# Kernel optimization log

Hardware: AMD Instinct MI355X
Metric: run time of the kernel (lower is better)

The kernel has to match this reference:

```python
import jax, jax.numpy as jnp
import numpy as np

DT = 0.2
LEN_HIST = 16
BATCH = 100000
LEN_PRED = 25


def _consts():
    H = jnp.zeros((2, 4), jnp.float32).at[0, 0].set(1.0).at[1, 2].set(1.0)
    Ht = H.T
    F = jnp.eye(4, dtype=jnp.float32).at[0, 1].set(DT).at[2, 3].set(DT)
    G = jnp.array([DT * DT / 2, DT, DT * DT / 2, DT], dtype=jnp.float32)
    Id = jnp.eye(4, dtype=jnp.float32)
    return H, Ht, F, G, Id


def setup_inputs():
    key = jax.random.key(0)
    hist = jax.random.normal(key, (LEN_HIST, BATCH, 2), dtype=jnp.float32)
    return {
        "hist": hist,
        "velocity_std_x": jnp.ones((1,), jnp.float32) * 0.1355,
        "velocity_std_y": jnp.ones((1,), jnp.float32) * 20.007,
        "acceleration_std_x": jnp.ones((1,), jnp.float32) * 2.771,
        "acceleration_std_y": jnp.ones((1,), jnp.float32) * 6.2014,
        "GR": jnp.array([1e-5, -1e-5], jnp.float32),
        "coef_G": jnp.array([-2.5296, 0.0723, -0.1533, -0.4032], jnp.float32),
        "len_pred": LEN_PRED,
    }


def _forward(hist, vsx, vsy, asx, asy, GR, coef_G, len_pred):
    H, Ht, F, G, Id = _consts()
    # Process noise Q: outer(G*tanh(coef_G)) with x/y diagonal blocks scaled
    ax2 = (asx * asx)[0]
    ay2 = (asy * asy)[0]
    mx = jnp.array([1.0, 1.0, 0.0, 0.0], jnp.float32)
    my = 1.0 - mx
    scale = ax2 * jnp.outer(mx, mx) + ay2 * jnp.outer(my, my) + jnp.outer(mx, my) + jnp.outer(my, mx)
    g = G * jnp.tanh(coef_G)
    Q = jnp.outer(g, g) * scale  # (4,4)
    R = jnp.outer(GR, GR)        # (2,2) measurement noise

    Z = hist[..., None]          # (T, B, 2, 1)
    B = hist.shape[1]

    # --- init ---
    V0 = (Z[1] - Z[0]) / DT                      # (B,2,1)
    X = Ht @ Z[0]                                # (B,4,1)
    X = X.at[:, 1, 0].set(V0[:, 0, 0]).at[:, 3, 0].set(V0[:, 1, 0])
    diag0 = jnp.stack([R[0, 0], (vsx * vsx)[0], R[1, 1], (vsy * vsy)[0]])
    P = jnp.broadcast_to(jnp.diag(diag0), (B, 4, 4))

    def pred(X, P):
        return F @ X, F @ P @ F.T + Q

    def filt_step(carry, z):
        X, P = carry
        X, P = pred(X, P)
        y = z - H @ X                            # (B,2,1)
        S = H @ P @ Ht + R                       # (B,2,2)
        # K = P H^T S^{-1}, computed as in torch.solve(H P^T, S^T)^T
        Kt = jnp.linalg.solve(jnp.swapaxes(S, -1, -2), H @ jnp.swapaxes(P, -1, -2))
        K = jnp.swapaxes(Kt, -1, -2)             # (B,4,2)
        X = X + K @ y
        ImKH = Id - K @ H
        P = ImKH @ P @ jnp.swapaxes(ImKH, -1, -2) + K @ R @ jnp.swapaxes(K, -1, -2)
        return (X, P), None

    (X, P), _ = jax.lax.scan(filt_step, (X, P), Z[1:])

    def pred_step(carry, _):
        X, P = pred(*carry)
        mu = (H @ X)[..., 0]                     # (B,2)
        Pout = H @ P @ Ht                        # (B,2,2)
        return (X, P), (mu, Pout)

    _, (mu, Pout) = jax.lax.scan(pred_step, (X, P), None, length=len_pred)
    sx = jnp.sqrt(Pout[..., 0, 0])[..., None]    # (L,B,1)
    sy = jnp.sqrt(Pout[..., 1, 1])[..., None]
    rho = (Pout[..., 0, 1] + Pout[..., 1, 0])[..., None] / (2.0 * sx * sy)
    return jnp.concatenate([mu, sx, sy, rho], axis=2)  # (L,B,5)


def reference(hist, velocity_std_x, velocity_std_y, acceleration_std_x, acceleration_std_y, GR, coef_G, len_pred):
    return _forward(hist, velocity_std_x, velocity_std_y, acceleration_std_x,
                    acceleration_std_y, GR, coef_G, len_pred)
```

## Files before the change

### kernel.cpp

```cpp
#include <hip/hip_runtime.h>
#include <math.h>

#define DT 0.2f
#define LEN_HIST 16

__global__ __launch_bounds__(256) void kalman_cv_kernel(
    const float* __restrict__ hist,
    const float* __restrict__ vsx_p, const float* __restrict__ vsy_p,
    const float* __restrict__ asx_p, const float* __restrict__ asy_p,
    const float* __restrict__ GR_p,  const float* __restrict__ coefG_p,
    float* __restrict__ out, int B, int len_pred)
{
    int b = blockIdx.x * blockDim.x + threadIdx.x;
    if (b >= B) return;

    const float Gv0 = DT * DT * 0.5f, Gv1 = DT, Gv2 = DT * DT * 0.5f, Gv3 = DT;
    float ax2 = asx_p[0] * asx_p[0];
    float ay2 = asy_p[0] * asy_p[0];
    float g[4];
    g[0] = Gv0 * tanhf(coefG_p[0]);
    g[1] = Gv1 * tanhf(coefG_p[1]);
    g[2] = Gv2 * tanhf(coefG_p[2]);
    g[3] = Gv3 * tanhf(coefG_p[3]);
    float Q[4][4];
    #pragma unroll
    for (int i = 0; i < 4; ++i) {
        #pragma unroll
        for (int j = 0; j < 4; ++j) {
            float s = (i < 2) ? ((j < 2) ? ax2 : 1.0f)
                              : ((j < 2) ? 1.0f : ay2);
            Q[i][j] = g[i] * g[j] * s;
        }
    }
    float GR0 = GR_p[0], GR1 = GR_p[1];
    float R00 = GR0 * GR0, R01 = GR0 * GR1, R10 = GR1 * GR0, R11 = GR1 * GR1;
    float vsx2 = vsx_p[0] * vsx_p[0];
    float vsy2 = vsy_p[0] * vsy_p[0];

    float2 z[LEN_HIST];
    #pragma unroll
    for (int t = 0; t < LEN_HIST; ++t)
        z[t] = *reinterpret_cast<const float2*>(hist + ((size_t)t * B + b) * 2);

    float X0 = z[0].x;
    float X1 = (z[1].x - z[0].x) / DT;
    float X2 = z[0].y;
    float X3 = (z[1].y - z[0].y) / DT;

    float P[4][4] = {};
    P[0][0] = R00; P[1][1] = vsx2; P[2][2] = R11; P[3][3] = vsy2;

    #pragma unroll
    for (int t = 1; t < LEN_HIST; ++t) {
        X0 += DT * X1;
        X2 += DT * X3;
        float T[4][4];
        #pragma unroll
        for (int j = 0; j < 4; ++j) {
            T[0][j] = P[0][j] + DT * P[1][j];
            T[1][j] = P[1][j];
            T[2][j] = P[2][j] + DT * P[3][j];
            T[3][j] = P[3][j];
        }
        #pragma unroll
        for (int i = 0; i < 4; ++i) {
            P[i][0] = T[i][0] + DT * T[i][1] + Q[i][0];
            P[i][1] = T[i][1]               + Q[i][1];
            P[i][2] = T[i][2] + DT * T[i][3] + Q[i][2];
            P[i][3] = T[i][3]               + Q[i][3];
        }

        float y0 = z[t].x - X0;
        float y1 = z[t].y - X2;
        float S00 = P[0][0] + R00, S01 = P[0][2] + R01;
        float S10 = P[2][0] + R10, S11 = P[2][2] + R11;
        float inv = 1.0f / (S00 * S11 - S01 * S10);
        float Si00 =  S11 * inv, Si01 = -S01 * inv;
        float Si10 = -S10 * inv, Si11 =  S00 * inv;

        float K[4][2];
        #pragma unroll
        for (int i = 0; i < 4; ++i) {
            K[i][0] = P[i][0] * Si00 + P[i][2] * Si10;
            K[i][1] = P[i][0] * Si01 + P[i][2] * Si11;
        }

        X0 += K[0][0] * y0 + K[0][1] * y1;
        X1 += K[1][0] * y0 + K[1][1] * y1;
        X2 += K[2][0] * y0 + K[2][1] * y1;
        X3 += K[3][0] * y0 + K[3][1] * y1;

        float U[4][4];
        #pragma unroll
        for (int i = 0; i < 4; ++i) {
            #pragma unroll
            for (int j = 0; j < 4; ++j)
                U[i][j] = P[i][j] - K[i][0] * P[0][j] - K[i][1] * P[2][j];
        }
        float w[4];
        #pragma unroll
        for (int i = 0; i < 4; ++i)
            w[i] = K[i][0] * GR0 + K[i][1] * GR1;
        #pragma unroll
        for (int i = 0; i < 4; ++i) {
            #pragma unroll
            for (int j = 0; j < 4; ++j)
                P[i][j] = U[i][j] - U[i][0] * K[j][0] - U[i][2] * K[j][1] + w[i] * w[j];
        }
    }

    size_t ob = (size_t)b * 5;
    for (int l = 0; l < len_pred; ++l) {
        X0 += DT * X1;
        X2 += DT * X3;
        float T[4][4];
        #pragma unroll
        for (int j = 0; j < 4; ++j) {
            T[0][j] = P[0][j] + DT * P[1][j];
            T[1][j] = P[1][j];
            T[2][j] = P[2][j] + DT * P[3][j];
            T[3][j] = P[3][j];
        }
        #pragma unroll
        for (int i = 0; i < 4; ++i) {
            P[i][0] = T[i][0] + DT * T[i][1] + Q[i][0];
            P[i][1] = T[i][1]               + Q[i][1];
            P[i][2] = T[i][2] + DT * T[i][3] + Q[i][2];
            P[i][3] = T[i][3]               + Q[i][3];
        }
        float sx = sqrtf(P[0][0]);
        float sy = sqrtf(P[2][2]);
        float rho = (P[0][2] + P[2][0]) / (2.0f * sx * sy);
        float* o = out + (size_t)l * B * 5 + ob;
        o[0] = X0;
        o[1] = X2;
        o[2] = sx;
        o[3] = sy;
        o[4] = rho;
    }
}

extern "C" void kernel_launch(void* const* d_in, const int* in_sizes, int n_in,
                              void* d_out, int out_size, void* d_ws, size_t ws_size,
                              hipStream_t stream) {
    const float* hist  = (const float*)d_in[0];
    const float* vsx   = (const float*)d_in[1];
    const float* vsy   = (const float*)d_in[2];
    const float* asx   = (const float*)d_in[3];
    const float* asy   = (const float*)d_in[4];
    const float* GR    = (const float*)d_in[5];
    const float* coefG = (const float*)d_in[6];
    float* out = (float*)d_out;

    int B = in_sizes[0] / (LEN_HIST * 2);
    int len_pred = out_size / (B * 5);

    int block = 256;
    int grid = (B + block - 1) / block;
    kalman_cv_kernel<<<grid, block, 0, stream>>>(hist, vsx, vsy, asx, asy, GR, coefG,
                                                 out, B, len_pred);
}
```

Measured before the change: 26.72 us.

## Exploit covariance symmetry and simplify Joseph update to reduce per-step ALU work

Stores the 4x4 covariance as its 10 unique upper-triangular entries and expands the F P F^T + Q product symbolically. The Joseph-form covariance update is replaced by the simple (I-KH)P form. Together these cut the FLOPs and register pressure of each filter and prediction step. The (I-KH)P form is mathematically equal only for the optimal gain and is less numerically robust, so results may drift slightly from the reference.

Measured after the change: 23.66 us. 1.13x faster.

```diff
diff --git a/kernel.cpp b/kernel.cpp
--- a/kernel.cpp
+++ b/kernel.cpp
@@ -3,140 +3,113 @@
 
 #define DT 0.2f
 #define LEN_HIST 16
+#define TPB 256
 
-__global__ __launch_bounds__(256) void kalman_cv_kernel(
+__global__ __launch_bounds__(TPB) void kalman_v4(
     const float* __restrict__ hist,
     const float* __restrict__ vsx_p, const float* __restrict__ vsy_p,
     const float* __restrict__ asx_p, const float* __restrict__ asy_p,
     const float* __restrict__ GR_p,  const float* __restrict__ coefG_p,
     float* __restrict__ out, int B, int len_pred)
 {
-    int b = blockIdx.x * blockDim.x + threadIdx.x;
+    const int b = blockIdx.x * TPB + threadIdx.x;
     if (b >= B) return;
-
-    const float Gv0 = DT * DT * 0.5f, Gv1 = DT, Gv2 = DT * DT * 0.5f, Gv3 = DT;
-    float ax2 = asx_p[0] * asx_p[0];
-    float ay2 = asy_p[0] * asy_p[0];
-    float g[4];
-    g[0] = Gv0 * tanhf(coefG_p[0]);
-    g[1] = Gv1 * tanhf(coefG_p[1]);
-    g[2] = Gv2 * tanhf(coefG_p[2]);
-    g[3] = Gv3 * tanhf(coefG_p[3]);
-    float Q[4][4];
-    #pragma unroll
-    for (int i = 0; i < 4; ++i) {
-        #pragma unroll
-        for (int j = 0; j < 4; ++j) {
-            float s = (i < 2) ? ((j < 2) ? ax2 : 1.0f)
-                              : ((j < 2) ? 1.0f : ay2);
-            Q[i][j] = g[i] * g[j] * s;
-        }
-    }
-    float GR0 = GR_p[0], GR1 = GR_p[1];
-    float R00 = GR0 * GR0, R01 = GR0 * GR1, R10 = GR1 * GR0, R11 = GR1 * GR1;
-    float vsx2 = vsx_p[0] * vsx_p[0];
-    float vsy2 = vsy_p[0] * vsy_p[0];
 
     float2 z[LEN_HIST];
     #pragma unroll
     for (int t = 0; t < LEN_HIST; ++t)
         z[t] = *reinterpret_cast<const float2*>(hist + ((size_t)t * B + b) * 2);
 
-    float X0 = z[0].x;
-    float X1 = (z[1].x - z[0].x) / DT;
-    float X2 = z[0].y;
-    float X3 = (z[1].y - z[0].y) / DT;
+    const float d = DT;
+    const float Gv0 = DT * DT * 0.5f, Gv1 = DT, Gv2 = DT * DT * 0.5f, Gv3 = DT;
+    const float ax2 = asx_p[0] * asx_p[0];
+    const float ay2 = asy_p[0] * asy_p[0];
+    const float g0 = Gv0 * tanhf(coefG_p[0]);
+    const float g1 = Gv1 * tanhf(coefG_p[1]);
+    const float g2 = Gv2 * tanhf(coefG_p[2]);
+    const float g3 = Gv3 * tanhf(coefG_p[3]);
+    const float Q00 = g0 * g0 * ax2, Q01 = g0 * g1 * ax2;
+    const float Q02 = g0 * g2,       Q03 = g0 * g3;
+    const float Q11 = g1 * g1 * ax2, Q12 = g1 * g2, Q13 = g1 * g3;
+    const float Q22 = g2 * g2 * ay2, Q23 = g2 * g3 * ay2, Q33 = g3 * g3 * ay2;
+    const float GR0 = GR_p[0], GR1 = GR_p[1];
+    const float R00 = GR0 * GR0, R01 = GR0 * GR1, R11 = GR1 * GR1;
 
-    float P[4][4] = {};
-    P[0][0] = R00; P[1][1] = vsx2; P[2][2] = R11; P[3][3] = vsy2;
+    float X0 = z[0].x, X1 = (z[1].x - z[0].x) / DT;
+    float X2 = z[0].y, X3 = (z[1].y - z[0].y) / DT;
+    float P00 = R00,                P01 = 0.f, P02 = 0.f, P03 = 0.f;
+    float P11 = vsx_p[0] * vsx_p[0], P12 = 0.f, P13 = 0.f;
+    float P22 = R11,                P23 = 0.f;
+    float P33 = vsy_p[0] * vsy_p[0];
 
     #pragma unroll
     for (int t = 1; t < LEN_HIST; ++t) {
-        X0 += DT * X1;
-        X2 += DT * X3;
-        float T[4][4];
-        #pragma unroll
-        for (int j = 0; j < 4; ++j) {
-            T[0][j] = P[0][j] + DT * P[1][j];
-            T[1][j] = P[1][j];
-            T[2][j] = P[2][j] + DT * P[3][j];
-            T[3][j] = P[3][j];
-        }
-        #pragma unroll
-        for (int i = 0; i < 4; ++i) {
-            P[i][0] = T[i][0] + DT * T[i][1] + Q[i][0];
-            P[i][1] = T[i][1]               + Q[i][1];
-            P[i][2] = T[i][2] + DT * T[i][3] + Q[i][2];
-            P[i][3] = T[i][3]               + Q[i][3];
-        }
+        const float n00 = P00 + d * (P01 + P01 + d * P11) + Q00;
+        const float n01 = P01 + d * P11 + Q01;
+        const float n02 = P02 + d * (P03 + P12 + d * P13) + Q02;
+        const float n03 = P03 + d * P13 + Q03;
+        const float n11 = P11 + Q11;
+        const float n12 = P12 + d * P13 + Q12;
+        const float n13 = P13 + Q13;
+        const float n22 = P22 + d * (P23 + P23 + d * P33) + Q22;
+        const float n23 = P23 + d * P33 + Q23;
+        const float n33 = P33 + Q33;
 
-        float y0 = z[t].x - X0;
-        float y1 = z[t].y - X2;
-        float S00 = P[0][0] + R00, S01 = P[0][2] + R01;
-        float S10 = P[2][0] + R10, S11 = P[2][2] + R11;
-        float inv = 1.0f / (S00 * S11 - S01 * S10);
-        float Si00 =  S11 * inv, Si01 = -S01 * inv;
-        float Si10 = -S10 * inv, Si11 =  S00 * inv;
+        X0 += d * X1; X2 += d * X3;
+        const float y0 = z[t].x - X0;
+        const float y1 = z[t].y - X2;
 
-        float K[4][2];
-        #pragma unroll
-        for (int i = 0; i < 4; ++i) {
-            K[i][0] = P[i][0] * Si00 + P[i][2] * Si10;
-            K[i][1] = P[i][0] * Si01 + P[i][2] * Si11;
-        }
+        const float S00 = n00 + R00, S01 = n02 + R01, S11 = n22 + R11;
+        const float inv = 1.0f / (S00 * S11 - S01 * S01);
+        const float Si00 = S11 * inv, Si01 = -S01 * inv, Si11 = S00 * inv;
 
-        X0 += K[0][0] * y0 + K[0][1] * y1;
-        X1 += K[1][0] * y0 + K[1][1] * y1;
-        X2 += K[2][0] * y0 + K[2][1] * y1;
-        X3 += K[3][0] * y0 + K[3][1] * y1;
+        const float K00 = n00 * Si00 + n02 * Si01, K01 = n00 * Si01 + n02 * Si11;
+        const float K10 = n01 * Si00 + n12 * Si01, K11 = n01 * Si01 + n12 * Si11;
+        const float K20 = n02 * Si00 + n22 * Si01, K21 = n02 * Si01 + n22 * Si11;
+        const float K30 = n03 * Si00 + n23 * Si01, K31 = n03 * Si01 + n23 * Si11;
 
-        float U[4][4];
-        #pragma unroll
-        for (int i = 0; i < 4; ++i) {
-            #pragma unroll
-            for (int j = 0; j < 4; ++j)
-                U[i][j] = P[i][j] - K[i][0] * P[0][j] - K[i][1] * P[2][j];
-        }
-        float w[4];
-        #pragma unroll
-        for (int i = 0; i < 4; ++i)
-            w[i] = K[i][0] * GR0 + K[i][1] * GR1;
-        #pragma unroll
-        for (int i = 0; i < 4; ++i) {
-            #pragma unroll
-            for (int j = 0; j < 4; ++j)
-                P[i][j] = U[i][j] - U[i][0] * K[j][0] - U[i][2] * K[j][1] + w[i] * w[j];
-        }
+        X0 += K00 * y0 + K01 * y1;
+        X1 += K10 * y0 + K11 * y1;
+        X2 += K20 * y0 + K21 * y1;
+        X3 += K30 * y0 + K31 * y1;
+
+        P00 = n00 - K00 * n00 - K01 * n02;
+        P01 = n01 - K00 * n01 - K01 * n12;
+        P02 = n02 - K00 * n02 - K01 * n22;
+        P03 = n03 - K00 * n03 - K01 * n23;
+        P11 = n11 - K10 * n01 - K11 * n12;
+        P12 = n12 - K10 * n02 - K11 * n22;
+        P13 = n13 - K10 * n03 - K11 * n23;
+        P22 = n22 - K20 * n02 - K21 * n22;
+        P23 = n23 - K20 * n03 - K21 * n23;
+        P33 = n33 - K30 * n03 - K31 * n23;
     }
 
-    size_t ob = (size_t)b * 5;
+    float* o = out + (size_t)b * 5;
+    const size_t ostride = (size_t)B * 5;
     for (int l = 0; l < len_pred; ++l) {
-        X0 += DT * X1;
-        X2 += DT * X3;
-        float T[4][4];
-        #pragma unroll
-        for (int j = 0; j < 4; ++j) {
-            T[0][j] = P[0][j] + DT * P[1][j];
-            T[1][j] = P[1][j];
-            T[2][j] = P[2][j] + DT * P[3][j];
-            T[3][j] = P[3][j];
-        }
-        #pragma unroll
-        for (int i = 0; i < 4; ++i) {
-            P[i][0] = T[i][0] + DT * T[i][1] + Q[i][0];
-            P[i][1] = T[i][1]               + Q[i][1];
-            P[i][2] = T[i][2] + DT * T[i][3] + Q[i][2];
-            P[i][3] = T[i][3]               + Q[i][3];
-        }
-        float sx = sqrtf(P[0][0]);
-        float sy = sqrtf(P[2][2]);
-        float rho = (P[0][2] + P[2][0]) / (2.0f * sx * sy);
-        float* o = out + (size_t)l * B * 5 + ob;
-        o[0] = X0;
-        o[1] = X2;
-        o[2] = sx;
-        o[3] = sy;
-        o[4] = rho;
+        const float n00 = P00 + d * (P01 + P01 + d * P11) + Q00;
+        const float n01 = P01 + d * P11 + Q01;
+        const float n02 = P02 + d * (P03 + P12 + d * P13) + Q02;
+        const float n03 = P03 + d * P13 + Q03;
+        const float n11 = P11 + Q11;
+        const float n12 = P12 + d * P13 + Q12;
+        const float n13 = P13 + Q13;
+        const float n22 = P22 + d * (P23 + P23 + d * P33) + Q22;
+        const float n23 = P23 + d * P33 + Q23;
+        const float n33 = P33 + Q33;
+        P00 = n00; P01 = n01; P02 = n02; P03 = n03;
+        P11 = n11; P12 = n12; P13 = n13;
+        P22 = n22; P23 = n23; P33 = n33;
+
+        X0 += d * X1; X2 += d * X3;
+
+        const float sx = sqrtf(P00);
+        const float sy = sqrtf(P22);
+        const float rho = P02 / (sx * sy);
+
+        o[0] = X0; o[1] = X2; o[2] = sx; o[3] = sy; o[4] = rho;
+        o += ostride;
     }
 }
 
@@ -155,8 +128,7 @@
     int B = in_sizes[0] / (LEN_HIST * 2);
     int len_pred = out_size / (B * 5);
 
-    int block = 256;
-    int grid = (B + block - 1) / block;
-    kalman_cv_kernel<<<grid, block, 0, stream>>>(hist, vsx, vsy, asx, asy, GR, coefG,
-                                                 out, B, len_pred);
+    int grid = (B + TPB - 1) / TPB;
+    kalman_v4<<<grid, TPB, 0, stream>>>(hist, vsx, vsy, asx, asy, GR, coefG,
+                                        out, B, len_pred);
 }
```
